# Kernel optimization log

Hardware: AMD Instinct MI355X
Metric: run time of the kernel (lower is better)

## Reference

```python
import jax, jax.numpy as jnp
import numpy as np

NPAT, NCON, E, H, L = 50000, 20000, 800000, 128, 2
DP, DC = 64, 128
N = NPAT + NCON  # homogeneous node count


def setup_inputs() -> dict:
    key = jax.random.key(0)
    k = jax.random.split(key, 12)
    s = 0.05
    return {
        "x_patient": jax.random.normal(k[0], (NPAT, DP), jnp.float32),
        "x_concept": jax.random.normal(k[1], (NCON, DC), jnp.float32),
        "W_p": jax.random.normal(k[2], (DP, H), jnp.float32) * s,
        "b_p": jnp.zeros((H,), jnp.float32),
        "W_c": jax.random.normal(k[3], (DC, H), jnp.float32) * s,
        "b_c": jnp.zeros((H,), jnp.float32),
        "W_root": jax.random.normal(k[4], (L, H, H), jnp.float32) * s,
        "b_root": jnp.zeros((L, H), jnp.float32),
        "W_rel": jax.random.normal(k[5], (L, 2, H, H), jnp.float32) * s,
        "src_pc": jax.random.randint(k[6], (E,), 0, NPAT),
        "dst_pc": jax.random.randint(k[7], (E,), 0, NCON),
        "src_cp": jax.random.randint(k[8], (E,), 0, NCON),
        "dst_cp": jax.random.randint(k[9], (E,), 0, NPAT),
    }


def reference(x_patient, x_concept, W_p, b_p, W_c, b_c, W_root, b_root, W_rel,
              src_pc, dst_pc, src_cp, dst_cp):
    # per-node-type linear projection, then concat into homogeneous graph
    # (patient offset 0, concept offset NPAT)
    x = jnp.concatenate([x_patient @ W_p + b_p, x_concept @ W_c + b_c], axis=0)  # [N, H]
    rel_edges = [(src_pc, dst_pc + NPAT), (src_cp + NPAT, dst_cp)]
    ones = jnp.ones((E,), jnp.float32)
    # per-relation in-degree for mean aggregation (zero-deg nodes -> 0 output)
    counts = [jnp.maximum(jax.ops.segment_sum(ones, d, num_segments=N), 1.0)[:, None]
              for _, d in rel_edges]
    for l in range(L):
        out = x @ W_root[l] + b_root[l]  # root transform + bias
        for r, (src, dst) in enumerate(rel_edges):
            msg = x[src] @ W_rel[l, r]  # [E, H] gather + relation transform
            out = out + jax.ops.segment_sum(msg, dst, num_segments=N) / counts[r]
        x = jax.nn.relu(out)
    return x  # [N, H]; rows [0:NPAT] are patient embeddings, rest concepts
```

## Files before the change

kernel.cpp:

```cpp
#include <hip/hip_runtime.h>
#include <hip/hip_bf16.h>

#define NPAT 50000
#define NCON 20000
#define NN   70000
#define EE   800000
#define H    128

#define NCON_AL  20032
#define SEGN     (NCON_AL + NPAT)
#define NBUCK    1095
#define RELSPLIT_B 313
#define BUCKCAP  5120
#define SUBS     16
#define SUBCAP   (BUCKCAP / SUBS)
#define BPE      4096
#define NBB      ((2 * EE + BPE - 1) / BPE)
#define CAP      4096
#define RMAX     8
#define NOFF     (64 * RMAX + 1)

typedef __attribute__((ext_vector_type(8))) short bf16x8;
typedef __attribute__((ext_vector_type(4))) float f32x4;

__device__ inline unsigned short f2bf(float f) {
    unsigned u = __float_as_uint(f);
    unsigned r = (u + 0x7FFFu + ((u >> 16) & 1u)) >> 16;
    return (unsigned short)r;
}
__device__ inline float bf2f_lo(unsigned v) { return __uint_as_float(v << 16); }
__device__ inline float bf2f_hi(unsigned v) { return __uint_as_float(v & 0xFFFF0000u); }

__device__ inline int bucket_of_block(int blk) {
    int p = blk / 7, r = blk % 7;
    if (r < 2) { int c = 2 * p + r; return (c < RELSPLIT_B) ? c : (NBUCK - 1); }
    return RELSPLIT_B + 5 * p + (r - 2);
}

__global__ void init_gcur_kernel(int* __restrict__ gcur) {
    int j = blockIdx.x * 256 + threadIdx.x;
    if (j < NBUCK * SUBS) gcur[j] = (j >> 4) * BUCKCAP + (j & (SUBS - 1)) * SUBCAP;
}

__global__ __launch_bounds__(512) void binpack_kernel(
        const int* __restrict__ dst_pc, const int* __restrict__ src_pc,
        const int* __restrict__ dst_cp, const int* __restrict__ src_cp,
        int* __restrict__ gcur, unsigned* __restrict__ pairs) {
    __shared__ unsigned sval[BPE];
    __shared__ unsigned short sbkt[BPE];
    __shared__ int cnt[NBUCK];
    __shared__ int delta[NBUCK];
    __shared__ int partial[512];
    int t = threadIdx.x, blk = blockIdx.x;
    int base = blk * BPE;
    int n = min(BPE, 2 * EE - base);

    for (int i = t; i < NBUCK; i += 512) cnt[i] = 0;
    __syncthreads();

    unsigned pay[8];
    int bkt[8];
#pragma unroll
    for (int q = 0; q < 8; q++) {
        int li = q * 512 + t;
        bkt[q] = -1;
        if (li < n) {
            int i = base + li;
            int seg, src;
            if (i < EE) { seg = dst_pc[i];                src = src_pc[i]; }
            else        { seg = NCON_AL + dst_cp[i - EE]; src = src_cp[i - EE]; }
            int b = seg >> 6;
            pay[q] = (unsigned)src | ((unsigned)(seg & 63) << 16);
            bkt[q] = b;
            atomicAdd(&cnt[b], 1);
        }
    }
    __syncthreads();

    const int PER = (NBUCK + 511) / 512;
    int beg = t * PER;
    int s = 0;
#pragma unroll
    for (int k = 0; k < PER; k++) { int i = beg + k; if (i < NBUCK) s += cnt[i]; }
    partial[t] = s;
    __syncthreads();
    for (int o = 1; o < 512; o <<= 1) {
        int v = (t >= o) ? partial[t - o] : 0;
        __syncthreads();
        partial[t] += v;
        __syncthreads();
    }
    int run = partial[t] - s;
    int sub = blk & (SUBS - 1);
    int prefk[PER];
#pragma unroll
    for (int k = 0; k < PER; k++) {
        int i = beg + k;
        if (i < NBUCK) {
            prefk[k] = run;
            int c = cnt[i];
            if (c > 0) {
                int gb = atomicAdd(&gcur[i * SUBS + sub], c);
                delta[i] = gb - run;
            }
            run += c;
        }
    }
    __syncthreads();
#pragma unroll
    for (int k = 0; k < PER; k++) { int i = beg + k; if (i < NBUCK) cnt[i] = prefk[k]; }
    __syncthreads();

#pragma unroll
    for (int q = 0; q < 8; q++) {
        if (bkt[q] >= 0) {
            int b = bkt[q];
            int pos = atomicAdd(&cnt[b], 1);
            sval[pos] = pay[q];
            sbkt[pos] = (unsigned short)b;
        }
    }
    __syncthreads();
    for (int i = t; i < n; i += 512)
        pairs[delta[sbkt[i]] + i] = sval[i];
}

__global__ __launch_bounds__(512) void build_ssrc_kernel(
        const unsigned* __restrict__ pairs, const int* __restrict__ gcur,
        int* __restrict__ soffg) {
    __shared__ int cnt[512];
    __shared__ int soff[NOFF];
    __shared__ int scur[512];
    __shared__ int wtot[8];
    __shared__ unsigned short ssrc[CAP];
    int t = threadIdx.x, b = bucket_of_block(blockIdx.x);
    int sh = (b < RELSPLIT_B) ? 13 : 12;
    cnt[t] = 0;
    __syncthreads();
    for (int s = 0; s < SUBS; s++) {
        int rbase = b * BUCKCAP + s * SUBCAP;
        int rcnt = gcur[b * SUBS + s] - rbase;
        for (int i = t; i < rcnt; i += 512) {
            unsigned p = pairs[rbase + i];
            atomicAdd(&cnt[(p >> 16) * RMAX + ((p & 0xFFFF) >> sh)], 1);
        }
    }
    __syncthreads();
    int wv = t >> 6, lane = t & 63;
    int v = cnt[t];
    int s = v;
#pragma unroll
    for (int o = 1; o < 64; o <<= 1) {
        int u = __shfl_up(s, o);
        if (lane >= o) s += u;
    }
    if (lane == 63) wtot[wv] = s;
    __syncthreads();
    if (t == 0) {
        int run = 0;
#pragma unroll
        for (int k = 0; k < 8; k++) { int tmp = wtot[k]; wtot[k] = run; run += tmp; }
    }
    __syncthreads();
    int incl = s + wtot[wv];
    soff[t + 1] = incl;
    if (t == 0) soff[0] = 0;
    scur[t] = incl - v;
    __syncthreads();
    for (int s2 = 0; s2 < SUBS; s2++) {
        int rbase = b * BUCKCAP + s2 * SUBCAP;
        int rcnt = gcur[b * SUBS + s2] - rbase;
        for (int i = t; i < rcnt; i += 512) {
            unsigned p = pairs[rbase + i];
            int pos = atomicAdd(&scur[(p >> 16) * RMAX + ((p & 0xFFFF) >> sh)], 1);
            ssrc[pos] = (unsigned short)(p & 0xFFFF);
        }
    }
    __syncthreads();
    for (int i = t; i < NOFF; i += 512) soffg[b * NOFF + i] = soff[i];
    int tot = soff[NOFF - 1];
    unsigned* sg = (unsigned*)(((unsigned short*)pairs) + (size_t)b * BUCKCAP * 2);
    const unsigned* sl = (const unsigned*)ssrc;
    for (int i = t; i < ((tot + 1) >> 1); i += 512) sg[i] = sl[i];
}

#define ACC8(a0, a1, v) \
    a0.x += bf2f_lo((v).x); a0.y += bf2f_hi((v).x); \
    a0.z += bf2f_lo((v).y); a0.w += bf2f_hi((v).y); \
    a1.x += bf2f_lo((v).z); a1.y += bf2f_hi((v).z); \
    a1.z += bf2f_lo((v).w); a1.w += bf2f_hi((v).w);

__global__ __launch_bounds__(512) void gather_kernel(
        const unsigned short* __restrict__ xbf,
        const unsigned short* __restrict__ ssrcg,
        const int* __restrict__ soffg,
        unsigned short* __restrict__ aggn) {
    __shared__ int soff[NOFF];
    __shared__ unsigned short ssrc[CAP];
    int t = threadIdx.x, b = bucket_of_block(blockIdx.x);
    for (int i = t; i < NOFF; i += 512) soff[i] = soffg[b * NOFF + i];
    __syncthreads();
    int tot = soff[NOFF - 1];
    const unsigned* sg = (const unsigned*)(ssrcg + (size_t)b * BUCKCAP * 2);
    unsigned* sl = (unsigned*)ssrc;
    for (int i = t; i < ((tot + 1) >> 1); i += 512) sl[i] = sg[i];
    __syncthreads();
    int wv = t >> 6, lane = t & 63;
    int g = lane >> 4;
    int q = lane & 15;
    int rowbase = (b < RELSPLIT_B) ? 0 : NPAT;
    int seglim  = (b < RELSPLIT_B) ? NCON : SEGN;
    const uint4* xw4 = (const uint4*)xbf;
    for (int i = 0; i < 8; i++) {
        int d = wv * 8 + i;
        int seg = b * 64 + d;
        if (seg >= seglim) continue;
        int beg = soff[d * RMAX], end = soff[(d + 1) * RMAX];
        float4 aA0 = {0.f, 0.f, 0.f, 0.f}, aA1 = {0.f, 0.f, 0.f, 0.f};
        float4 aB0 = {0.f, 0.f, 0.f, 0.f}, aB1 = {0.f, 0.f, 0.f, 0.f};
        int j = beg;
        for (; j + 7 < end; j += 8) {
            int sA = ssrc[j + g];
            int sB = ssrc[j + 4 + g];
            uint4 vA = xw4[(size_t)(rowbase + sA) * 16 + q];
            uint4 vB = xw4[(size_t)(rowbase + sB) * 16 + q];
            ACC8(aA0, aA1, vA);
            ACC8(aB0, aB1, vB);
        }
        for (; j < end; j += 4) {
            if (g < end - j) {
                int s0 = ssrc[j + g];
                uint4 v = xw4[(size_t)(rowbase + s0) * 16 + q];
                ACC8(aA0, aA1, v);
            }
        }
        aA0.x += aB0.x; aA0.y += aB0.y; aA0.z += aB0.z; aA0.w += aB0.w;
        aA1.x += aB1.x; aA1.y += aB1.y; aA1.z += aB1.z; aA1.w += aB1.w;
        float r0 = aA0.x, r1 = aA0.y, r2 = aA0.z, r3 = aA0.w;
        float r4 = aA1.x, r5 = aA1.y, r6 = aA1.z, r7 = aA1.w;
        r0 += __shfl_xor(r0, 16); r1 += __shfl_xor(r1, 16);
        r2 += __shfl_xor(r2, 16); r3 += __shfl_xor(r3, 16);
        r4 += __shfl_xor(r4, 16); r5 += __shfl_xor(r5, 16);
        r6 += __shfl_xor(r6, 16); r7 += __shfl_xor(r7, 16);
        r0 += __shfl_xor(r0, 32); r1 += __shfl_xor(r1, 32);
        r2 += __shfl_xor(r2, 32); r3 += __shfl_xor(r3, 32);
        r4 += __shfl_xor(r4, 32); r5 += __shfl_xor(r5, 32);
        r6 += __shfl_xor(r6, 32); r7 += __shfl_xor(r7, 32);
        if (g == 0) {
            float inv = 1.0f / (float)max(end - beg, 1);
            uint4 o;
            o.x = (unsigned)f2bf(r0 * inv) | ((unsigned)f2bf(r1 * inv) << 16);
            o.y = (unsigned)f2bf(r2 * inv) | ((unsigned)f2bf(r3 * inv) << 16);
            o.z = (unsigned)f2bf(r4 * inv) | ((unsigned)f2bf(r5 * inv) << 16);
            o.w = (unsigned)f2bf(r6 * inv) | ((unsigned)f2bf(r7 * inv) << 16);
            *(uint4*)&aggn[(size_t)seg * H + 8 * q] = o;
        }
    }
}

#define BM 128
#define BK 8

struct GemmJob {
    const float* A1;
    const float* B1;
    const float* bias; unsigned short* Cbf;
    int lda1, K1, M;
};

__global__ void gemm_dual_kernel(GemmJob j0, GemmJob j1, int nb0) {
    __shared__ float sA[BK][BM];
    __shared__ float sB[BK][H];
    bool first = (int)blockIdx.x < nb0;
    GemmJob j = first ? j0 : j1;
    int bm = (first ? blockIdx.x : blockIdx.x - nb0) * BM;
    int tid = threadIdx.x;
    int am = tid >> 1;
    int ak = (tid & 1) * 4;
    int bk = tid >> 5;
    int bn = (tid & 31) * 4;
    int ty = tid >> 4;
    int tx = tid & 15;
    float acc[8][8] = {};
    for (int k0 = 0; k0 < j.K1; k0 += BK) {
        int gm = bm + am; if (gm >= j.M) gm = j.M - 1;
        float4 av = *(const float4*)&j.A1[(size_t)gm * j.lda1 + k0 + ak];
        float4 bv = *(const float4*)&j.B1[(size_t)(k0 + bk) * H + bn];
        __syncthreads();
        sA[ak + 0][am] = av.x; sA[ak + 1][am] = av.y;
        sA[ak + 2][am] = av.z; sA[ak + 3][am] = av.w;
        *(float4*)&sB[bk][bn] = bv;
        __syncthreads();
#pragma unroll
        for (int k = 0; k < BK; k++) {
            float a[8], bb[8];
            *(float4*)&a[0] = *(const float4*)&sA[k][ty * 8];
            *(float4*)&a[4] = *(const float4*)&sA[k][ty * 8 + 4];
            *(float4*)&bb[0] = *(const float4*)&sB[k][tx * 4];
            *(float4*)&bb[4] = *(const float4*)&sB[k][64 + tx * 4];
#pragma unroll
            for (int i = 0; i < 8; i++)
#pragma unroll
                for (int jj = 0; jj < 8; jj++)
                    acc[i][jj] += a[i] * bb[jj];
        }
    }
    float bcol[8];
    *(float4*)&bcol[0] = *(const float4*)&j.bias[tx * 4];
    *(float4*)&bcol[4] = *(const float4*)&j.bias[64 + tx * 4];
#pragma unroll
    for (int i = 0; i < 8; i++) {
        int gr = bm + ty * 8 + i;
        if (gr < j.M) {
#pragma unroll
            for (int q = 0; q < 8; q++) {
                float v = acc[i][q] + bcol[q];
                int gc = (q < 4) ? (tx * 4 + q) : (64 + tx * 4 + q - 4);
                j.Cbf[(size_t)gr * H + gc] = f2bf(v);
            }
        }
    }
}

struct MJob {
    const unsigned short* A1;
    const unsigned short* A2;
    const float* B1;
    const float* B2;
    const float* bias;
    float* C;
    unsigned short* Cbf;
    int M;
};

__global__ __launch_bounds__(256) void gemm_mfma_kernel(MJob j0, MJob j1, int nb0) {
    __shared__ unsigned short sA[128][40];
    __shared__ unsigned short sBT[128][40];
    bool first = (int)blockIdx.x < nb0;
    MJob J = first ? j0 : j1;
    int bm = (first ? (int)blockIdx.x : (int)blockIdx.x - nb0) * 128;
    int tid = threadIdx.x;
    int wv = tid >> 6, lane = tid & 63;
    int wr = wv >> 1, wc = wv & 1;
    int m16 = lane & 15, kg = lane >> 4;

    f32x4 acc[4][4];
#pragma unroll
    for (int a = 0; a < 4; a++)
#pragma unroll
        for (int c = 0; c < 4; c++) acc[a][c] = (f32x4){0.f, 0.f, 0.f, 0.f};

    int ar = tid >> 1, ah = tid & 1;
    int gmA = bm + ar; if (gmA >= J.M) gmA = J.M - 1;
    int bn = tid & 127, bk0 = tid >> 7;

#pragma unroll
    for (int kt = 0; kt < 8; kt++) {
        int k0 = kt * 32;
        const unsigned short* asrc = (k0 < 128)
            ? (J.A1 + (size_t)gmA * H + k0)
            : (J.A2 + (size_t)gmA * H + (k0 - 128));
        const uint4* a4 = (const uint4*)(asrc + ah * 16);
        uint4 av0 = a4[0], av1 = a4[1];
        const float* bsrc = (k0 < 128) ? (J.B1 + (size_t)k0 * H)
                                       : (J.B2 + (size_t)(k0 - 128) * H);
        float bvals[16];
#pragma unroll
        for (int kk = 0; kk < 16; kk++) bvals[kk] = bsrc[(size_t)(2 * kk + bk0) * H + bn];
        __syncthreads();
        { uint4* d4 = (uint4*)&sA[ar][ah * 16]; d4[0] = av0; d4[1] = av1; }
#pragma unroll
        for (int kk = 0; kk < 16; kk++) sBT[bn][2 * kk + bk0] = f2bf(bvals[kk]);
        __syncthreads();
        bf16x8 af[4], bfg[4];
#pragma unroll
        for (int mt = 0; mt < 4; mt++)
            af[mt] = *(bf16x8*)&sA[wr * 64 + mt * 16 + m16][kg * 8];
#pragma unroll
        for (int nt = 0; nt < 4; nt++)
            bfg[nt] = *(bf16x8*)&sBT[wc * 64 + nt * 16 + m16][kg * 8];
#pragma unroll
        for (int mt = 0; mt < 4; mt++)
#pragma unroll
            for (int nt = 0; nt < 4; nt++)
                acc[mt][nt] = __builtin_amdgcn_mfma_f32_16x16x32_bf16(
                    af[mt], bfg[nt], acc[mt][nt], 0, 0, 0);
    }
    float bv[4];
#pragma unroll
    for (int nt = 0; nt < 4; nt++) bv[nt] = J.bias[wc * 64 + nt * 16 + m16];
#pragma unroll
    for (int mt = 0; mt < 4; mt++) {
        int gr0 = bm + wr * 64 + mt * 16 + kg * 4;
#pragma unroll
        for (int r = 0; r < 4; r++) {
            int gr = gr0 + r;
            if (gr < J.M) {
#pragma unroll
                for (int nt = 0; nt < 4; nt++) {
                    int gc = wc * 64 + nt * 16 + m16;
                    float v = fmaxf(acc[mt][nt][r] + bv[nt], 0.f);
                    if (J.C)   J.C[(size_t)gr * H + gc] = v;
                    if (J.Cbf) J.Cbf[(size_t)gr * H + gc] = f2bf(v);
                }
            }
        }
    }
}


extern "C" void kernel_launch(void* const* d_in, const int* in_sizes, int n_in,
                              void* d_out, int out_size, void* d_ws, size_t ws_size,
                              hipStream_t stream) {
    const float* x_patient = (const float*)d_in[0];
    const float* x_concept = (const float*)d_in[1];
    const float* W_p       = (const float*)d_in[2];
    const float* b_p       = (const float*)d_in[3];
    const float* W_c       = (const float*)d_in[4];
    const float* b_c       = (const float*)d_in[5];
    const float* W_root    = (const float*)d_in[6];
    const float* b_root    = (const float*)d_in[7];
    const float* W_rel     = (const float*)d_in[8];
    const int*   src_pc    = (const int*)d_in[9];
    const int*   dst_pc    = (const int*)d_in[10];
    const int*   src_cp    = (const int*)d_in[11];
    const int*   dst_cp    = (const int*)d_in[12];
    float* out = (float*)d_out;

    char* w = (char*)d_ws;
    unsigned short* xbf  = (unsigned short*)w; w += (size_t)NN * H * 2;
    unsigned short* aggn = (unsigned short*)w; w += (size_t)SEGN * H * 2;
    int* gcur = (int*)w;            w += (size_t)NBUCK * SUBS * 4;
    unsigned* pairs = (unsigned*)w; w += (size_t)NBUCK * BUCKCAP * 4;
    int* soffg = (int*)w;           w += (size_t)NBUCK * NOFF * 4;

    init_gcur_kernel<<<(NBUCK * SUBS + 255) / 256, 256, 0, stream>>>(gcur);
    binpack_kernel<<<NBB, 512, 0, stream>>>(dst_pc, src_pc, dst_cp, src_cp, gcur, pairs);
    build_ssrc_kernel<<<NBUCK, 512, 0, stream>>>(pairs, gcur, soffg);
    const unsigned short* ssrcg = (const unsigned short*)pairs;

    const int PB = (NPAT + BM - 1) / BM;
    const int CB = (NCON + BM - 1) / BM;

    {
        GemmJob jp = { x_patient, W_p, b_p, xbf, 64, 64, NPAT };
        GemmJob jc = { x_concept, W_c, b_c, xbf + (size_t)NPAT * H, 128, 128, NCON };
        gemm_dual_kernel<<<PB + CB, 256, 0, stream>>>(jp, jc, PB);
    }

    for (int l = 0; l < 2; l++) {
        gather_kernel<<<NBUCK, 512, 0, stream>>>(xbf, ssrcg, soffg, aggn);
        const float* Wroot_l = W_root + (size_t)l * H * H;
        const float* Wrel_l0 = W_rel + (size_t)(l * 2 + 0) * H * H;
        const float* Wrel_l1 = W_rel + (size_t)(l * 2 + 1) * H * H;
        const float* br = b_root + (size_t)l * H;
        float* cp = (l == 1) ? out : nullptr;
        float* cc = (l == 1) ? out + (size_t)NPAT * H : nullptr;
        unsigned short* bp = (l == 0) ? xbf : nullptr;
        unsigned short* bc = (l == 0) ? xbf + (size_t)NPAT * H : nullptr;
        MJob jp = { xbf, aggn + (size_t)NCON_AL * H, Wroot_l, Wrel_l1, br,
                    cp, bp, NPAT };
        MJob jc = { xbf + (size_t)NPAT * H, aggn, Wroot_l, Wrel_l0, br,
                    cc, bc, NCON };
        gemm_mfma_kernel<<<PB + CB, 256, 0, stream>>>(jp, jc, PB);
    }
}
```

Before: 324.7 us.

## Fuse input projection GEMM into CSR build kernel and simplify binpack scan

Merges the input projection GEMM and the per-bucket CSR build into one launch: the first blocks run the projection with a smaller per-thread tile at 512 threads, and the rest build the sorted source lists, with shared memory overlaid through a union. The binpack block scan now uses wavefront shuffles instead of a barrier-heavy shared-memory Hillis-Steele loop. The interleaved bucket-to-block mapping that balanced the two relation types across blocks is dropped in favour of identity order. This saves a launch and lets the two independent phases overlap, but the union raises shared-memory usage for the GEMM blocks and may lower their occupancy.

```diff
diff --git a/kernel.cpp b/kernel.cpp
--- a/kernel.cpp
+++ b/kernel.cpp
@@ -20,6 +20,9 @@
 #define RMAX     8
 #define NOFF     (64 * RMAX + 1)
 
+#define BM 128
+#define BK 8
+
 typedef __attribute__((ext_vector_type(8))) short bf16x8;
 typedef __attribute__((ext_vector_type(4))) float f32x4;
 
@@ -30,12 +33,6 @@
 }
 __device__ inline float bf2f_lo(unsigned v) { return __uint_as_float(v << 16); }
 __device__ inline float bf2f_hi(unsigned v) { return __uint_as_float(v & 0xFFFF0000u); }
-
-__device__ inline int bucket_of_block(int blk) {
-    int p = blk / 7, r = blk % 7;
-    if (r < 2) { int c = 2 * p + r; return (c < RELSPLIT_B) ? c : (NBUCK - 1); }
-    return RELSPLIT_B + 5 * p + (r - 2);
-}
 
 __global__ void init_gcur_kernel(int* __restrict__ gcur) {
     int j = blockIdx.x * 256 + threadIdx.x;
@@ -50,7 +47,7 @@
     __shared__ unsigned short sbkt[BPE];
     __shared__ int cnt[NBUCK];
     __shared__ int delta[NBUCK];
-    __shared__ int partial[512];
+    __shared__ int wtot[8];
     int t = threadIdx.x, blk = blockIdx.x;
     int base = blk * BPE;
     int n = min(BPE, 2 * EE - base);
@@ -82,15 +79,23 @@
     int s = 0;
 #pragma unroll
     for (int k = 0; k < PER; k++) { int i = beg + k; if (i < NBUCK) s += cnt[i]; }
-    partial[t] = s;
-    __syncthreads();
-    for (int o = 1; o < 512; o <<= 1) {
-        int v = (t >= o) ? partial[t - o] : 0;
-        __syncthreads();
-        partial[t] += v;
-        __syncthreads();
-    }
-    int run = partial[t] - s;
+    int lane = t & 63, w8 = t >> 6;
+    int incl = s;
+#pragma unroll
+    for (int o = 1; o < 64; o <<= 1) {
+        int u = __shfl_up(incl, o);
+        if (lane >= o) incl += u;
+    }
+    if (lane == 63) wtot[w8] = incl;
+    __syncthreads();
+    if (t == 0) {
+        int r0 = 0;
+#pragma unroll
+        for (int k = 0; k < 8; k++) { int tmp = wtot[k]; wtot[k] = r0; r0 += tmp; }
+    }
+    __syncthreads();
+    int run = incl - s + wtot[w8];
+
     int sub = blk & (SUBS - 1);
     int prefk[PER];
 #pragma unroll
@@ -125,62 +130,133 @@
         pairs[delta[sbkt[i]] + i] = sval[i];
 }
 
-__global__ __launch_bounds__(512) void build_ssrc_kernel(
+
+struct GemmJob {
+    const float* A1;
+    const float* B1;
+    const float* bias; unsigned short* Cbf;
+    int lda1, K1, M;
+};
+
+union FusedSmem {
+    struct {
+        int cnt[512];
+        int soff[NOFF];
+        int scur[512];
+        int wtot[8];
+        unsigned short ssrc[CAP];
+    } b;
+    struct {
+        float sA[BK][BM];
+        float sB[BK][H];
+    } p;
+};
+
+__global__ __launch_bounds__(512) void build_proj_kernel(
         const unsigned* __restrict__ pairs, const int* __restrict__ gcur,
-        int* __restrict__ soffg) {
-    __shared__ int cnt[512];
-    __shared__ int soff[NOFF];
-    __shared__ int scur[512];
-    __shared__ int wtot[8];
-    __shared__ unsigned short ssrc[CAP];
-    int t = threadIdx.x, b = bucket_of_block(blockIdx.x);
+        int* __restrict__ soffg, GemmJob j0, GemmJob j1, int nb0, int nproj) {
+    __shared__ FusedSmem sm;
+    int t = threadIdx.x;
+    int blk = blockIdx.x;
+
+    if (blk < nproj) {
+        bool first = blk < nb0;
+        GemmJob j = first ? j0 : j1;
+        int bm = (first ? blk : blk - nb0) * BM;
+        int ar = t >> 2;
+        int ac = (t & 3) * 2;
+        int bk = t >> 6;
+        int bn = (t & 63) * 2;
+        int ty = t >> 4;
+        int tx = t & 15;
+        float acc[4][8] = {};
+        int gm = bm + ar; if (gm >= j.M) gm = j.M - 1;
+        for (int k0 = 0; k0 < j.K1; k0 += BK) {
+            float2 av = *(const float2*)&j.A1[(size_t)gm * j.lda1 + k0 + ac];
+            float2 bv = *(const float2*)&j.B1[(size_t)(k0 + bk) * H + bn];
+            __syncthreads();
+            sm.p.sA[ac + 0][ar] = av.x; sm.p.sA[ac + 1][ar] = av.y;
+            *(float2*)&sm.p.sB[bk][bn] = bv;
+            __syncthreads();
+#pragma unroll
+            for (int k = 0; k < BK; k++) {
+                float a[4], bb[8];
+                *(float4*)&a[0] = *(const float4*)&sm.p.sA[k][ty * 4];
+                *(float4*)&bb[0] = *(const float4*)&sm.p.sB[k][tx * 4];
+                *(float4*)&bb[4] = *(const float4*)&sm.p.sB[k][64 + tx * 4];
+#pragma unroll
+                for (int i = 0; i < 4; i++)
+#pragma unroll
+                    for (int jj = 0; jj < 8; jj++)
+                        acc[i][jj] += a[i] * bb[jj];
+            }
+        }
+        float bcol[8];
+        *(float4*)&bcol[0] = *(const float4*)&j.bias[tx * 4];
+        *(float4*)&bcol[4] = *(const float4*)&j.bias[64 + tx * 4];
+#pragma unroll
+        for (int i = 0; i < 4; i++) {
+            int gr = bm + ty * 4 + i;
+            if (gr < j.M) {
+#pragma unroll
+                for (int q = 0; q < 8; q++) {
+                    float v = acc[i][q] + bcol[q];
+                    int gc = (q < 4) ? (tx * 4 + q) : (64 + tx * 4 + q - 4);
+                    j.Cbf[(size_t)gr * H + gc] = f2bf(v);
+                }
+            }
+        }
+        return;
+    }
+
+    int b = blk - nproj;
     int sh = (b < RELSPLIT_B) ? 13 : 12;
-    cnt[t] = 0;
+    sm.b.cnt[t] = 0;
     __syncthreads();
     for (int s = 0; s < SUBS; s++) {
         int rbase = b * BUCKCAP + s * SUBCAP;
         int rcnt = gcur[b * SUBS + s] - rbase;
         for (int i = t; i < rcnt; i += 512) {
             unsigned p = pairs[rbase + i];
-            atomicAdd(&cnt[(p >> 16) * RMAX + ((p & 0xFFFF) >> sh)], 1);
+            atomicAdd(&sm.b.cnt[(p >> 16) * RMAX + ((p & 0xFFFF) >> sh)], 1);
         }
     }
     __syncthreads();
     int wv = t >> 6, lane = t & 63;
-    int v = cnt[t];
+    int v = sm.b.cnt[t];
     int s = v;
 #pragma unroll
     for (int o = 1; o < 64; o <<= 1) {
         int u = __shfl_up(s, o);
         if (lane >= o) s += u;
     }
-    if (lane == 63) wtot[wv] = s;
+    if (lane == 63) sm.b.wtot[wv] = s;
     __syncthreads();
     if (t == 0) {
         int run = 0;
 #pragma unroll
-        for (int k = 0; k < 8; k++) { int tmp = wtot[k]; wtot[k] = run; run += tmp; }
-    }
-    __syncthreads();
-    int incl = s + wtot[wv];
-    soff[t + 1] = incl;
-    if (t == 0) soff[0] = 0;
-    scur[t] = incl - v;
+        for (int k = 0; k < 8; k++) { int tmp = sm.b.wtot[k]; sm.b.wtot[k] = run; run += tmp; }
+    }
+    __syncthreads();
+    int incl = s + sm.b.wtot[wv];
+    sm.b.soff[t + 1] = incl;
+    if (t == 0) sm.b.soff[0] = 0;
+    sm.b.scur[t] = incl - v;
     __syncthreads();
     for (int s2 = 0; s2 < SUBS; s2++) {
         int rbase = b * BUCKCAP + s2 * SUBCAP;
         int rcnt = gcur[b * SUBS + s2] - rbase;
         for (int i = t; i < rcnt; i += 512) {
             unsigned p = pairs[rbase + i];
-            int pos = atomicAdd(&scur[(p >> 16) * RMAX + ((p & 0xFFFF) >> sh)], 1);
-            ssrc[pos] = (unsigned short)(p & 0xFFFF);
-        }
-    }
-    __syncthreads();
-    for (int i = t; i < NOFF; i += 512) soffg[b * NOFF + i] = soff[i];
-    int tot = soff[NOFF - 1];
+            int pos = atomicAdd(&sm.b.scur[(p >> 16) * RMAX + ((p & 0xFFFF) >> sh)], 1);
+            sm.b.ssrc[pos] = (unsigned short)(p & 0xFFFF);
+        }
+    }
+    __syncthreads();
+    for (int i = t; i < NOFF; i += 512) soffg[b * NOFF + i] = sm.b.soff[i];
+    int tot = sm.b.soff[NOFF - 1];
     unsigned* sg = (unsigned*)(((unsigned short*)pairs) + (size_t)b * BUCKCAP * 2);
-    const unsigned* sl = (const unsigned*)ssrc;
+    const unsigned* sl = (const unsigned*)sm.b.ssrc;
     for (int i = t; i < ((tot + 1) >> 1); i += 512) sg[i] = sl[i];
 }
 
@@ -197,7 +273,7 @@
         unsigned short* __restrict__ aggn) {
     __shared__ int soff[NOFF];
     __shared__ unsigned short ssrc[CAP];
-    int t = threadIdx.x, b = bucket_of_block(blockIdx.x);
+    int t = threadIdx.x, b = blockIdx.x;
     for (int i = t; i < NOFF; i += 512) soff[i] = soffg[b * NOFF + i];
     __syncthreads();
     int tot = soff[NOFF - 1];
@@ -258,70 +334,6 @@
     }
 }
 
-#define BM 128
-#define BK 8
-
-struct GemmJob {
-    const float* A1;
-    const float* B1;
-    const float* bias; unsigned short* Cbf;
-    int lda1, K1, M;
-};
-
-__global__ void gemm_dual_kernel(GemmJob j0, GemmJob j1, int nb0) {
-    __shared__ float sA[BK][BM];
-    __shared__ float sB[BK][H];
-    bool first = (int)blockIdx.x < nb0;
-    GemmJob j = first ? j0 : j1;
-    int bm = (first ? blockIdx.x : blockIdx.x - nb0) * BM;
-    int tid = threadIdx.x;
-    int am = tid >> 1;
-    int ak = (tid & 1) * 4;
-    int bk = tid >> 5;
-    int bn = (tid & 31) * 4;
-    int ty = tid >> 4;
-    int tx = tid & 15;
-    float acc[8][8] = {};
-    for (int k0 = 0; k0 < j.K1; k0 += BK) {
-        int gm = bm + am; if (gm >= j.M) gm = j.M - 1;
-        float4 av = *(const float4*)&j.A1[(size_t)gm * j.lda1 + k0 + ak];
-        float4 bv = *(const float4*)&j.B1[(size_t)(k0 + bk) * H + bn];
-        __syncthreads();
-        sA[ak + 0][am] = av.x; sA[ak + 1][am] = av.y;
-        sA[ak + 2][am] = av.z; sA[ak + 3][am] = av.w;
-        *(float4*)&sB[bk][bn] = bv;
-        __syncthreads();
-#pragma unroll
-        for (int k = 0; k < BK; k++) {
-            float a[8], bb[8];
-            *(float4*)&a[0] = *(const float4*)&sA[k][ty * 8];
-            *(float4*)&a[4] = *(const float4*)&sA[k][ty * 8 + 4];
-            *(float4*)&bb[0] = *(const float4*)&sB[k][tx * 4];
-            *(float4*)&bb[4] = *(const float4*)&sB[k][64 + tx * 4];
-#pragma unroll
-            for (int i = 0; i < 8; i++)
-#pragma unroll
-                for (int jj = 0; jj < 8; jj++)
-                    acc[i][jj] += a[i] * bb[jj];
-        }
-    }
-    float bcol[8];
-    *(float4*)&bcol[0] = *(const float4*)&j.bias[tx * 4];
-    *(float4*)&bcol[4] = *(const float4*)&j.bias[64 + tx * 4];
-#pragma unroll
-    for (int i = 0; i < 8; i++) {
-        int gr = bm + ty * 8 + i;
-        if (gr < j.M) {
-#pragma unroll
-            for (int q = 0; q < 8; q++) {
-                float v = acc[i][q] + bcol[q];
-                int gc = (q < 4) ? (tx * 4 + q) : (64 + tx * 4 + q - 4);
-                j.Cbf[(size_t)gr * H + gc] = f2bf(v);
-            }
-        }
-    }
-}
-
 struct MJob {
     const unsigned short* A1;
     const unsigned short* A2;
@@ -434,19 +446,20 @@
     unsigned* pairs = (unsigned*)w; w += (size_t)NBUCK * BUCKCAP * 4;
     int* soffg = (int*)w;           w += (size_t)NBUCK * NOFF * 4;
 
+    const int PB = (NPAT + BM - 1) / BM;
+    const int CB = (NCON + BM - 1) / BM;
+    const int NPROJ = PB + CB;
+
     init_gcur_kernel<<<(NBUCK * SUBS + 255) / 256, 256, 0, stream>>>(gcur);
     binpack_kernel<<<NBB, 512, 0, stream>>>(dst_pc, src_pc, dst_cp, src_cp, gcur, pairs);
-    build_ssrc_kernel<<<NBUCK, 512, 0, stream>>>(pairs, gcur, soffg);
-    const unsigned short* ssrcg = (const unsigned short*)pairs;
-
-    const int PB = (NPAT + BM - 1) / BM;
-    const int CB = (NCON + BM - 1) / BM;
 
     {
         GemmJob jp = { x_patient, W_p, b_p, xbf, 64, 64, NPAT };
         GemmJob jc = { x_concept, W_c, b_c, xbf + (size_t)NPAT * H, 128, 128, NCON };
-        gemm_dual_kernel<<<PB + CB, 256, 0, stream>>>(jp, jc, PB);
-    }
+        build_proj_kernel<<<NPROJ + NBUCK, 512, 0, stream>>>(
+            pairs, gcur, soffg, jp, jc, PB, NPROJ);
+    }
+    const unsigned short* ssrcg = (const unsigned short*)pairs;
 
     for (int l = 0; l < 2; l++) {
         gather_kernel<<<NBUCK, 512, 0, stream>>>(xbf, ssrcg, soffg, aggn);
```

After: 319.7 us. No clear change (-1.5%).
